# Kernel tuning notes

Hardware: AMD Instinct MI355X
Metric: run time of the kernel (lower is better)

Reference implementation:

```python
import jax, jax.numpy as jnp
import numpy as np

NUM_HEADS = 12   # top-k = num_heads experts selected per token
SWITCHLOSS = 0.1
ZLOSS = 0.001


def setup_inputs() -> dict:
    key = jax.random.key(0)
    ks = jax.random.split(key, 8)
    B, N, C, E, D = 2, 2048, 768, 24, 64
    w = lambda k, shape: (jax.random.normal(k, shape, jnp.float32) * 0.02)
    return {
        "x": jax.random.normal(ks[0], (B, N, C), jnp.float32),
        "w_gate": w(ks[1], (C, E)),
        "W_in": w(ks[2], (E, C, D)),    # per-expert q projection
        "b_in": jnp.zeros((E, D), jnp.float32),
        "W_out": w(ks[3], (E, D, C)),   # per-expert output projection
        "b_out": jnp.zeros((E, C), jnp.float32),
        "W_kv": w(ks[4], (C, 2 * D)),   # shared single-head K/V
        "b_kv": jnp.zeros((2 * D,), jnp.float32),
    }


def reference(x, w_gate, W_in, b_in, W_out, b_out, W_kv, b_kv):
    B, N, C = x.shape
    E, _, D = W_in.shape
    H = NUM_HEADS
    scale = D ** -0.5

    xf = x.reshape(-1, C)                         # [T, C], T = B*N
    # --- top-k gating (k = num_heads) ---
    logits = xf @ w_gate                          # [T, E]
    probs = jax.nn.softmax(logits, axis=-1)
    top_p, idx = jax.lax.top_k(probs, H)          # [T, H]
    gates = top_p / (top_p.sum(-1, keepdims=True) + 1e-6)
    oh = jax.nn.one_hot(idx, E, dtype=x.dtype)    # [T, H, E]
    comb = oh * gates[..., None]                  # gated dispatch/combine weights

    # --- aux losses (switchloss + zloss; cvloss coeff = 0) ---
    dense_gates = comb.sum(1)                     # [T, E]
    freqs = (dense_gates > 0).astype(x.dtype).sum(0)
    p_sum = probs.sum(0)
    switch = E * jnp.sum((p_sum / p_sum.sum()) * (freqs / freqs.sum()))
    z = jnp.mean(jax.nn.logsumexp(logits, axis=1) ** 2)
    aux_loss = SWITCHLOSS * switch + ZLOSS * z

    # --- MoE map: per-token q via selected experts (no gate multiply) ---
    q_all = jnp.einsum('tc,ecd->ted', xf, W_in) + b_in     # [T, E, D]
    q = jnp.take_along_axis(q_all, idx[..., None], axis=1)  # [T, H, D]
    q = q.reshape(B, N, H, D)

    # --- shared-KV attention (multi-query style) ---
    kv = x @ W_kv + b_kv
    k, v = jnp.split(kv, 2, axis=-1)              # [B, N, D] each
    attn = jnp.einsum('bihd,bjd->bhij', q, k) * scale
    attn = jax.nn.softmax(attn, axis=-1)
    o = jnp.einsum('bhij,bjd->bihd', attn, v).reshape(-1, H, D)  # [T, H, D]

    # --- MoE reduce: gated combine through per-expert output projections ---
    xe = jnp.einsum('the,thd->ted', comb, o)      # [T, E, D] gated dispatch
    out = jnp.einsum('ted,edc->tc', xe, W_out) + jnp.einsum('the,ec->tc', comb, b_out)
    return out.reshape(B, N, C), aux_loss
```

## Files before the change

### kernel.cpp

```cpp
#include <hip/hip_runtime.h>
#include <hip/hip_bf16.h>

#define T_  4096
#define Bb  2
#define Nn  2048
#define Cc  768
#define Ee  24
#define Dd  64
#define Hh  12
#define KR  1568
#define KS  16
#define KC  48
#define NB2 1024
#define SCL 0.18033688f

typedef __attribute__((ext_vector_type(8))) short bf16x8;
typedef __attribute__((ext_vector_type(4))) short bf16x4;
typedef __attribute__((ext_vector_type(4))) float f32x4;

__device__ __forceinline__ unsigned short f2bf(float f) {
  union { float f; unsigned int i; } u; u.f = f;
  unsigned int r = u.i + 0x7FFFu + ((u.i >> 16) & 1u);
  return (unsigned short)(r >> 16);
}
__device__ __forceinline__ float bf2f(unsigned short s) {
  union { unsigned int i; float f; } u; u.i = ((unsigned int)s) << 16; return u.f;
}

__device__ __forceinline__ void gload16(const void* g, void* l) {
  __builtin_amdgcn_global_load_lds(
      (const __attribute__((address_space(1))) void*)g,
      (__attribute__((address_space(3))) void*)l, 16, 0, 0);
}

__global__ __launch_bounds__(256) void convert_all_kernel(
    const float* __restrict__ W_in, const float* __restrict__ W_out,
    const float* __restrict__ b_out, const float* __restrict__ W_kv,
    unsigned short* __restrict__ BqT, unsigned short* __restrict__ BrT,
    unsigned short* __restrict__ BkvT)
{
  __shared__ float ls[64 * 129];
  const int bid = blockIdx.x, tid = threadIdx.x;
  if (bid < 288) {
    const int e = bid / 12, c0 = (bid % 12) * 64;
    #pragma unroll
    for (int i = 0; i < 16; ++i) {
      int L = tid + i * 256, c = L >> 6, d = L & 63;
      ls[c * 65 + d] = W_in[(size_t)e * Cc * Dd + (size_t)(c0 + c) * Dd + d];
    }
    __syncthreads();
    #pragma unroll
    for (int i = 0; i < 16; ++i) {
      int L = tid + i * 256, d = L >> 6, c = L & 63;
      BqT[(size_t)(e * Dd + d) * Cc + c0 + c] = f2bf(ls[c * 65 + d]);
    }
  } else if (bid < 876) {
    const int i2 = bid - 288;
    const int k0 = (i2 / 12) * 32, n0 = (i2 % 12) * 64;
    #pragma unroll
    for (int i = 0; i < 8; ++i) {
      int L = tid + i * 256, k = L >> 6, n = L & 63;
      int kk = k0 + k;
      float v = (kk < 1536) ? W_out[(size_t)kk * Cc + n0 + n]
              : (kk < 1560) ? b_out[(size_t)(kk - 1536) * Cc + n0 + n] : 0.f;
      ls[k * 65 + n] = v;
    }
    __syncthreads();
    #pragma unroll
    for (int i = 0; i < 8; ++i) {
      int L = tid + i * 256, n = L >> 5, k = L & 31;
      BrT[(size_t)(n0 + n) * KR + k0 + k] = f2bf(ls[k * 65 + n]);
    }
  } else {
    const int c0 = (bid - 876) * 64;
    #pragma unroll
    for (int i = 0; i < 32; ++i) {
      int L = tid + i * 256, c = L >> 7, j = L & 127;
      ls[c * 129 + j] = W_kv[(size_t)(c0 + c) * 128 + j];
    }
    __syncthreads();
    #pragma unroll
    for (int i = 0; i < 32; ++i) {
      int L = tid + i * 256, j = L >> 6, c = L & 63;
      BkvT[(size_t)j * Cc + c0 + c] = f2bf(ls[c * 129 + j]);
    }
  }
}

template<int MODE, int BM>
__global__ __launch_bounds__(256) void gemm_bt_kernel(
    const unsigned short* __restrict__ A, const unsigned short* __restrict__ BT,
    const float* __restrict__ bias, const float* __restrict__ bias2,
    void* __restrict__ Cout, void* __restrict__ Cout2, void* __restrict__ Cout3,
    int K, int ldc)
{
  constexpr int MI = BM / 32;
  __shared__ __align__(16) unsigned short As[BM * 32];
  __shared__ __align__(16) unsigned short Bs[128 * 32];
  const int tid = threadIdx.x, w = tid >> 6, lane = tid & 63;
  const int quad = lane >> 4, nl = lane & 15;
  const int m0 = blockIdx.x * BM, n0 = blockIdx.y * 128;
  const int mw = (w & 1) * (BM / 2), nw = (w >> 1) * 64;

  f32x4 acc[MI][4];
  #pragma unroll
  for (int i = 0; i < MI; ++i)
    #pragma unroll
    for (int j = 0; j < 4; ++j) acc[i][j] = (f32x4){0.f, 0.f, 0.f, 0.f};

  const int rlane = lane >> 2, col8 = (lane & 3) * 8;
  const int row0a = w * (BM / 4) + rlane;
  const int row0b = w * 32 + rlane;
  const unsigned short* a0 = A + (size_t)(m0 + row0a) * K + col8;
  const unsigned short* a1 = a0 + (size_t)16 * K;
  const unsigned short* b0 = BT + (size_t)(n0 + row0b) * K + col8;
  const unsigned short* b1 = b0 + (size_t)16 * K;
  unsigned short* lA0 = As + (w * (BM / 4)) * 32;
  unsigned short* lA1 = As + (w * (BM / 4) + 16) * 32;
  unsigned short* lB0 = Bs + (w * 32) * 32;
  unsigned short* lB1 = Bs + (w * 32 + 16) * 32;

  for (int k0 = 0; k0 < K; k0 += 32) {
    gload16(a0 + k0, lA0);
    if (BM == 128) gload16(a1 + k0, lA1);
    gload16(b0 + k0, lB0);
    gload16(b1 + k0, lB1);
    __syncthreads();

    bf16x8 af[MI], bfr[4];
    #pragma unroll
    for (int mi = 0; mi < MI; ++mi)
      af[mi] = *(const bf16x8*)&As[(mw + mi * 16 + nl) * 32 + quad * 8];
    #pragma unroll
    for (int ni = 0; ni < 4; ++ni)
      bfr[ni] = *(const bf16x8*)&Bs[(nw + ni * 16 + nl) * 32 + quad * 8];
    #pragma unroll
    for (int mi = 0; mi < MI; ++mi)
      #pragma unroll
      for (int ni = 0; ni < 4; ++ni)
        acc[mi][ni] = __builtin_amdgcn_mfma_f32_16x16x32_bf16(
            af[mi], bfr[ni], acc[mi][ni], 0, 0, 0);
    __syncthreads();
  }

  #pragma unroll
  for (int mi = 0; mi < MI; ++mi) {
    int rowb = m0 + mw + mi * 16 + quad * 4;
    int bb = rowb >> 11, nn = rowb & (Nn - 1);
    #pragma unroll
    for (int ni = 0; ni < 4; ++ni) {
      int col = n0 + nw + ni * 16 + nl;
      if (MODE == 0) {
        #pragma unroll
        for (int reg = 0; reg < 4; ++reg)
          ((float*)Cout)[(size_t)(rowb + reg) * ldc + col] = acc[mi][ni][reg];
      } else {
        if (col < 1536) {
          float bv = bias[col];
          #pragma unroll
          for (int reg = 0; reg < 4; ++reg)
            ((unsigned short*)Cout)[(size_t)(rowb + reg) * 1536 + col] =
                f2bf((acc[mi][ni][reg] + bv) * SCL);
        } else {
          int c2 = col - 1536;
          float bv = bias2[c2];
          if (c2 < Dd) {
            #pragma unroll
            for (int reg = 0; reg < 4; ++reg)
              ((unsigned short*)Cout2)[((size_t)bb * Nn + nn + reg) * Dd + c2] =
                  f2bf(acc[mi][ni][reg] + bv);
          } else {
            int p6 = nn & 63;
            int np = (nn & ~63) | (p6 & 0x23)
                   | (((p6 >> 4) & 1) << 2) | (((p6 >> 2) & 3) << 3);
            ushort4 v;
            v.x = f2bf(acc[mi][ni][0] + bv);
            v.y = f2bf(acc[mi][ni][1] + bv);
            v.z = f2bf(acc[mi][ni][2] + bv);
            v.w = f2bf(acc[mi][ni][3] + bv);
            *(ushort4*)((unsigned short*)Cout3 +
                        ((size_t)bb * Dd + (c2 - Dd)) * Nn + np) = v;
          }
        }
      }
    }
  }
}

#define XPAD 52
__global__ __launch_bounds__(256) void gate1_kernel(
    const float* __restrict__ x, const float* __restrict__ wg,
    float* __restrict__ partial, unsigned short* __restrict__ xb)
{
  __shared__ __align__(16) float xs[256 * XPAD];
  __shared__ __align__(16) float wsT[Ee * KC];
  const int tid = threadIdx.x;
  const int t0 = blockIdx.x * 256;
  const int s = blockIdx.y, k0 = s * KC;

  #pragma unroll
  for (int i = 0; i < 12; ++i) {
    int f = tid + i * 256;
    int token = f / 12, j = f % 12;
    size_t gofs = (size_t)(t0 + token) * Cc + k0 + j * 4;
    float4 v = *(const float4*)&x[gofs];
    *(float4*)&xs[token * XPAD + j * 4] = v;
    ushort4 o;
    o.x = f2bf(v.x); o.y = f2bf(v.y); o.z = f2bf(v.z); o.w = f2bf(v.w);
    *(ushort4*)&xb[gofs] = o;
  }
  for (int i = tid; i < Ee * KC; i += 256)
    wsT[(i % Ee) * KC + i / Ee] = wg[k0 * Ee + i];
  __syncthreads();

  float xr[KC];
  #pragma unroll
  for (int kg = 0; kg < KC / 4; ++kg)
    *(float4*)&xr[kg * 4] = *(const float4*)&xs[tid * XPAD + kg * 4];

  float acc[Ee];
  #pragma unroll
  for (int e = 0; e < Ee; ++e) acc[e] = 0.f;
  #pragma unroll
  for (int e = 0; e < Ee; ++e) {
    #pragma unroll
    for (int kg = 0; kg < KC / 4; ++kg) {
      float4 wv = *(const float4*)&wsT[e * KC + kg * 4];
      acc[e] += xr[kg * 4 + 0] * wv.x + xr[kg * 4 + 1] * wv.y
              + xr[kg * 4 + 2] * wv.z + xr[kg * 4 + 3] * wv.w;
    }
  }

  float* dst = partial + ((size_t)(t0 + tid) * KS + s) * Ee;
  #pragma unroll
  for (int eg = 0; eg < Ee / 4; ++eg)
    *(float4*)&dst[eg * 4] = *(float4*)&acc[eg * 4];
}

__global__ __launch_bounds__(256) void gate2_kernel(
    const float* __restrict__ partial,
    int* __restrict__ idx, float* __restrict__ gate, float* __restrict__ bstats)
{
  __shared__ float xls[4][KS * Ee];
  __shared__ float sacc[49];
  const int tid = threadIdx.x;
  const int w = tid >> 6, lane = tid & 63;
  const int t = blockIdx.x * 4 + w;

  if (tid < 49) sacc[tid] = 0.f;

  const float* p = partial + (size_t)t * (KS * Ee);
  #pragma unroll
  for (int i = 0; i < 6; ++i) xls[w][lane + i * 64] = p[lane + i * 64];

  float logit = -1e30f;
  if (lane < Ee) {
    float acc = 0.f;
    #pragma unroll
    for (int s = 0; s < KS; ++s) acc += xls[w][s * Ee + lane];
    logit = acc;
  }
  float m = logit;
  for (int o = 32; o; o >>= 1) m = fmaxf(m, __shfl_xor(m, o));
  float pr = (lane < Ee) ? expf(logit - m) : 0.f;
  float s = pr;
  for (int o = 32; o; o >>= 1) s += __shfl_xor(s, o);
  float prob = pr / s;
  float lse = m + logf(s);

  bool sel = false;
  float my_p = 0.f; int my_e = -1;
  for (int h = 0; h < Hh; ++h) {
    float v = (lane < Ee && !sel) ? prob : -1.f;
    int ix = lane;
    for (int o = 32; o; o >>= 1) {
      float ov = __shfl_xor(v, o); int oi = __shfl_xor(ix, o);
      if (ov > v || (ov == v && oi < ix)) { v = ov; ix = oi; }
    }
    if (lane == ix) sel = true;
    if (lane == h) { my_p = v; my_e = ix; }
  }
  float gsum = (lane < Hh) ? my_p : 0.f;
  for (int o = 32; o; o >>= 1) gsum += __shfl_xor(gsum, o);
  if (lane < Hh) {
    idx[t * Hh + lane] = my_e;
    gate[t * Hh + lane] = my_p / (gsum + 1e-6f);
  }

  __syncthreads();
  if (lane < Ee) atomicAdd(&sacc[lane], prob);
  if (lane < Hh) atomicAdd(&sacc[24 + my_e], 1.0f);
  if (lane == 0) atomicAdd(&sacc[48], lse * lse);
  __syncthreads();
  if (tid < 49) bstats[(size_t)tid * NB2 + blockIdx.x] = sacc[tid];
}

__global__ __launch_bounds__(256) void attn_kernel(
    const unsigned short* __restrict__ qallb, const int* __restrict__ idx,
    const unsigned short* __restrict__ kbuf, const unsigned short* __restrict__ vtbuf,
    float* __restrict__ opart, float* __restrict__ lpart)
{
  __shared__ __align__(16) unsigned short ksl[64 * 64];
  __shared__ __align__(16) unsigned short vtl[64 * 64];

  const int tid = threadIdx.x;
  const int w = tid >> 6, lane = tid & 63;
  const int quad = lane >> 4, nl = lane & 15;
  const int bh = blockIdx.y;
  const int b = bh / Hh, h = bh - b * Hh;
  const int qw = blockIdx.x * 128 + w * 32;
  const int sp = blockIdx.z;
  const int jbeg = sp * (Nn / 2);

  bf16x8 qB0[2], qB1[2];
  #pragma unroll
  for (int g = 0; g < 2; ++g) {
    const int tq = b * Nn + qw + g * 16 + nl;
    const int eq = idx[tq * Hh + h];
    const unsigned short* qrow = qallb + (size_t)tq * (Ee * Dd) + eq * Dd + quad * 8;
    qB0[g] = *(const bf16x8*)(qrow);
    qB1[g] = *(const bf16x8*)(qrow + 32);
  }

  f32x4 acc[2][4];
  #pragma unroll
  for (int g = 0; g < 2; ++g)
    #pragma unroll
    for (int dg = 0; dg < 4; ++dg) acc[g][dg] = (f32x4){0.f, 0.f, 0.f, 0.f};
  float l[2] = {0.f, 0.f};

  const int sr  = lane >> 3;
  const int cbd = (lane & 7) ^ sr;
  const int xl  = nl & 7;
  const int ca0 = (quad ^ xl) * 8;
  const int ca1 = ((quad + 4) ^ xl) * 8;

  for (int j0 = jbeg; j0 < jbeg + Nn / 2; j0 += 64) {
    #pragma unroll
    for (int i = 0; i < 2; ++i) {
      int r = w * 16 + i * 8;
      gload16(kbuf + ((size_t)b * Nn + j0 + r + sr) * Dd + cbd * 8, ksl + r * 64);
      gload16(vtbuf + ((size_t)b * Dd + r + sr) * Nn + j0 + cbd * 8, vtl + r * 64);
    }
    __syncthreads();

    bf16x4 pf[2][4];
    #pragma unroll
    for (int kg = 0; kg < 4; ++kg) {
      const unsigned short* kr = ksl + (kg * 16 + nl) * 64;
      bf16x8 a0 = *(const bf16x8*)(kr + ca0);
      bf16x8 a1 = *(const bf16x8*)(kr + ca1);
      #pragma unroll
      for (int g = 0; g < 2; ++g) {
        f32x4 c = {0.f, 0.f, 0.f, 0.f};
        c = __builtin_amdgcn_mfma_f32_16x16x32_bf16(a0, qB0[g], c, 0, 0, 0);
        c = __builtin_amdgcn_mfma_f32_16x16x32_bf16(a1, qB1[g], c, 0, 0, 0);
        float p0 = __builtin_amdgcn_exp2f(c[0]);
        float p1 = __builtin_amdgcn_exp2f(c[1]);
        float p2 = __builtin_amdgcn_exp2f(c[2]);
        float p3 = __builtin_amdgcn_exp2f(c[3]);
        l[g] += (p0 + p1) + (p2 + p3);
        union { __hip_bfloat162 h2[2]; bf16x4 v; } pk;
        pk.h2[0] = __float22bfloat162_rn(float2{p0, p1});
        pk.h2[1] = __float22bfloat162_rn(float2{p2, p3});
        pf[g][kg] = pk.v;
      }
    }
    bf16x8 pb[2][2];
    #pragma unroll
    for (int g = 0; g < 2; ++g) {
      pb[g][0] = __builtin_shufflevector(pf[g][0], pf[g][1], 0, 1, 2, 3, 4, 5, 6, 7);
      pb[g][1] = __builtin_shufflevector(pf[g][2], pf[g][3], 0, 1, 2, 3, 4, 5, 6, 7);
    }
    #pragma unroll
    for (int dg = 0; dg < 4; ++dg) {
      const unsigned short* vrow = vtl + (dg * 16 + nl) * 64;
      bf16x8 v0 = *(const bf16x8*)(vrow + ca0);
      bf16x8 v1 = *(const bf16x8*)(vrow + ca1);
      #pragma unroll
      for (int g = 0; g < 2; ++g) {
        acc[g][dg] = __builtin_amdgcn_mfma_f32_16x16x32_bf16(v0, pb[g][0], acc[g][dg], 0, 0, 0);
        acc[g][dg] = __builtin_amdgcn_mfma_f32_16x16x32_bf16(v1, pb[g][1], acc[g][dg], 0, 0, 0);
      }
    }
    __syncthreads();
  }

  #pragma unroll
  for (int g = 0; g < 2; ++g) {
    float lg = l[g];
    lg += __shfl_xor(lg, 16);
    lg += __shfl_xor(lg, 32);
    if (lane < 16)
      lpart[(size_t)sp * (Bb * Hh * Nn) + (size_t)bh * Nn + qw + g * 16 + nl] = lg;
    float* orow = opart + (size_t)sp * ((size_t)Bb * Hh * Nn * Dd)
                + ((size_t)bh * Nn + qw + g * 16 + nl) * Dd + quad * 4;
    #pragma unroll
    for (int dg = 0; dg < 4; ++dg) {
      float4 o;
      o.x = acc[g][dg][0]; o.y = acc[g][dg][1];
      o.z = acc[g][dg][2]; o.w = acc[g][dg][3];
      *(float4*)(orow + dg * 16) = o;
    }
  }
}

__global__ __launch_bounds__(256) void scatter_kernel(
    const float* __restrict__ opart, const float* __restrict__ lpart,
    const int* __restrict__ idx, const float* __restrict__ gate,
    unsigned short* __restrict__ xeg)
{
  __shared__ int   sel[Ee];
  __shared__ float glh[Hh];
  __shared__ float gg[Hh];
  const int t = blockIdx.x, b = t >> 11, nn = t & (Nn - 1);
  const int tid = threadIdx.x;
  const size_t HN = (size_t)Bb * Hh * Nn;
  if (tid < Ee) sel[tid] = -1;
  __syncthreads();
  if (tid < Hh) {
    int e = idx[t * Hh + tid];
    sel[e] = tid;
    float g = gate[t * Hh + tid];
    gg[tid] = g;
    size_t row = (size_t)(b * Hh + tid) * Nn + nn;
    glh[tid] = g / (lpart[row] + lpart[HN + row]);
  }
  __syncthreads();
  for (int c = tid; c < KR; c += 256) {
    float v = 0.f;
    if (c < 1536) {
      int e = c >> 6, h = sel[e];
      if (h >= 0) {
        size_t oofs = ((size_t)(b * Hh + h) * Nn + nn) * Dd + (c & 63);
        v = glh[h] * (opart[oofs] + opart[HN * Dd + oofs]);
      }
    } else if (c < 1560) {
      int h = sel[c - 1536];
      if (h >= 0) v = gg[h];
    }
    xeg[(size_t)t * KR + c] = f2bf(v);
  }
}

__global__ __launch_bounds__(256) void aux1_kernel(
    const float* __restrict__ bstats, float* __restrict__ stats2)
{
  __shared__ float r[4];
  const int j = blockIdx.x, tid = threadIdx.x;
  float4 v = *(const float4*)&bstats[(size_t)j * NB2 + tid * 4];
  float s = (v.x + v.y) + (v.z + v.w);
  for (int o = 32; o; o >>= 1) s += __shfl_xor(s, o);
  if ((tid & 63) == 0) r[tid >> 6] = s;
  __syncthreads();
  if (tid == 0) stats2[j] = (r[0] + r[1]) + (r[2] + r[3]);
}

__global__ void aux2_kernel(const float* __restrict__ stats2,
                            float* __restrict__ out, int out_size)
{
  const int lane = threadIdx.x;
  float a = (lane < Ee) ? stats2[lane] : 0.f;
  float b = (lane < Ee) ? stats2[24 + lane] : 0.f;
  float pt = a, ft = b, sw = a * b;
  for (int o = 32; o; o >>= 1) {
    pt += __shfl_xor(pt, o); ft += __shfl_xor(ft, o); sw += __shfl_xor(sw, o);
  }
  if (lane == 0) {
    float sswitch = (float)Ee * sw / (pt * ft);
    float z = stats2[48] * (1.0f / (float)T_);
    out[out_size - 1] = 0.1f * sswitch + 0.001f * z;
  }
}

extern "C" void kernel_launch(void* const* d_in, const int* in_sizes, int n_in,
                              void* d_out, int out_size, void* d_ws, size_t ws_size,
                              hipStream_t stream)
{
  const float* x     = (const float*)d_in[0];
  const float* wg    = (const float*)d_in[1];
  const float* W_in  = (const float*)d_in[2];
  const float* b_in  = (const float*)d_in[3];
  const float* W_out = (const float*)d_in[4];
  const float* b_out = (const float*)d_in[5];
  const float* W_kv  = (const float*)d_in[6];
  const float* b_kv  = (const float*)d_in[7];
  float* out = (float*)d_out;

  char* ws = (char*)d_ws;
  size_t off = 0;
  auto carve = [&](size_t bytes) -> void* {
    void* p = ws + off;
    off = (off + bytes + 255) & ~(size_t)255;
    return p;
  };
  int*            idx    = (int*)           carve((size_t)T_ * Hh * 4);
  float*          gate   = (float*)         carve((size_t)T_ * Hh * 4);
  float*          bstats = (float*)         carve((size_t)49 * NB2 * 4);
  float*          stats2 = (float*)         carve(256);
  float*          lpart  = (float*)         carve((size_t)2 * Bb * Hh * Nn * 4);
  float*          lgate  = (float*)         carve((size_t)T_ * KS * Ee * 4);
  unsigned short* xb     = (unsigned short*)carve((size_t)T_ * Cc * 2);
  unsigned short* BqkvT  = (unsigned short*)carve((size_t)(Ee * Dd + 128) * Cc * 2);
  unsigned short* BkvT   = BqkvT + (size_t)Ee * Dd * Cc;
  unsigned short* BrT    = (unsigned short*)carve((size_t)Cc * KR * 2);
  unsigned short* kbuf   = (unsigned short*)carve((size_t)T_ * Dd * 2);
  unsigned short* vtbuf  = (unsigned short*)carve((size_t)T_ * Dd * 2);
  unsigned short* qallb  = (unsigned short*)carve((size_t)T_ * Ee * Dd * 2);
  float*          opart  = (float*)         carve((size_t)2 * Bb * Hh * Nn * Dd * 4);
  unsigned short* xeg    = (unsigned short*)carve((size_t)T_ * KR * 2);

  convert_all_kernel<<<888, 256, 0, stream>>>(
      W_in, W_out, b_out, W_kv, BqkvT, BrT, BkvT);

  gate1_kernel<<<dim3(T_ / 256, KS), 256, 0, stream>>>(x, wg, lgate, xb);
  gate2_kernel<<<NB2, 256, 0, stream>>>(lgate, idx, gate, bstats);

  gemm_bt_kernel<1, 64><<<dim3(T_ / 64, 13), 256, 0, stream>>>(
      xb, BqkvT, b_in, b_kv, qallb, kbuf, vtbuf, Cc, 1536);

  attn_kernel<<<dim3(Nn / 128, Bb * Hh, 2), 256, 0, stream>>>(
      qallb, idx, kbuf, vtbuf, opart, lpart);

  scatter_kernel<<<T_, 256, 0, stream>>>(opart, lpart, idx, gate, xeg);

  gemm_bt_kernel<0, 64><<<dim3(T_ / 64, Cc / 128), 256, 0, stream>>>(
      xeg, BrT, nullptr, nullptr, out, nullptr, nullptr, KR, Cc);

  aux1_kernel<<<49, 256, 0, stream>>>(bstats, stats2);
  aux2_kernel<<<1, 64, 0, stream>>>(stats2, out, out_size);
}
```

Before: 215.3 us.

## Triple-buffer K/V tiles in attention and enlarge GEMM row tiles

The attention kernel now keeps three LDS buffers for K and V^T tiles. It issues asynchronous loads two tiles ahead and waits on partial vmcnt counts, so global loads overlap MFMA compute. It also raises wave priority during compute and sets launch bounds to 3 blocks per CU. Separately, both GEMM launches switch to 128-row tiles, which halves the grid size and gives more reuse per block, at the cost of fewer blocks and more LDS and registers.

```diff
diff --git a/kernel.cpp b/kernel.cpp
--- a/kernel.cpp
+++ b/kernel.cpp
@@ -295,13 +295,13 @@
   if (tid < 49) bstats[(size_t)tid * NB2 + blockIdx.x] = sacc[tid];
 }
 
-__global__ __launch_bounds__(256) void attn_kernel(
+__global__ __launch_bounds__(256, 3) void attn_kernel(
     const unsigned short* __restrict__ qallb, const int* __restrict__ idx,
     const unsigned short* __restrict__ kbuf, const unsigned short* __restrict__ vtbuf,
     float* __restrict__ opart, float* __restrict__ lpart)
 {
-  __shared__ __align__(16) unsigned short ksl[64 * 64];
-  __shared__ __align__(16) unsigned short vtl[64 * 64];
+  __shared__ __align__(16) unsigned short ksl[3][64 * 64];
+  __shared__ __align__(16) unsigned short vtl[3][64 * 64];
 
   const int tid = threadIdx.x;
   const int w = tid >> 6, lane = tid & 63;
@@ -310,7 +310,7 @@
   const int b = bh / Hh, h = bh - b * Hh;
   const int qw = blockIdx.x * 128 + w * 32;
   const int sp = blockIdx.z;
-  const int jbeg = sp * (Nn / 2);
+  const int T0 = sp * 16;
 
   bf16x8 qB0[2], qB1[2];
   #pragma unroll
@@ -335,19 +335,26 @@
   const int ca0 = (quad ^ xl) * 8;
   const int ca1 = ((quad + 4) ^ xl) * 8;
 
-  for (int j0 = jbeg; j0 < jbeg + Nn / 2; j0 += 64) {
+  const unsigned short* kgbase =
+      kbuf + ((size_t)b * Nn + w * 16 + sr) * Dd + cbd * 8;
+  const unsigned short* vgbase =
+      vtbuf + ((size_t)b * Dd + w * 16 + sr) * Nn + cbd * 8;
+
+  auto STAGE = [&](int bi, int t) {
+    const int j0 = t * 64;
     #pragma unroll
     for (int i = 0; i < 2; ++i) {
-      int r = w * 16 + i * 8;
-      gload16(kbuf + ((size_t)b * Nn + j0 + r + sr) * Dd + cbd * 8, ksl + r * 64);
-      gload16(vtbuf + ((size_t)b * Dd + r + sr) * Nn + j0 + cbd * 8, vtl + r * 64);
-    }
-    __syncthreads();
-
+      gload16(kgbase + (size_t)(j0 + i * 8) * Dd, &ksl[bi][(w * 16 + i * 8) * 64]);
+      gload16(vgbase + (size_t)(i * 8) * Nn + j0, &vtl[bi][(w * 16 + i * 8) * 64]);
+    }
+  };
+
+  auto COMPUTE = [&](const unsigned short* ks_, const unsigned short* vt_) {
+    __builtin_amdgcn_s_setprio(1);
     bf16x4 pf[2][4];
     #pragma unroll
     for (int kg = 0; kg < 4; ++kg) {
-      const unsigned short* kr = ksl + (kg * 16 + nl) * 64;
+      const unsigned short* kr = ks_ + (kg * 16 + nl) * 64;
       bf16x8 a0 = *(const bf16x8*)(kr + ca0);
       bf16x8 a1 = *(const bf16x8*)(kr + ca1);
       #pragma unroll
@@ -374,7 +381,7 @@
     }
     #pragma unroll
     for (int dg = 0; dg < 4; ++dg) {
-      const unsigned short* vrow = vtl + (dg * 16 + nl) * 64;
+      const unsigned short* vrow = vt_ + (dg * 16 + nl) * 64;
       bf16x8 v0 = *(const bf16x8*)(vrow + ca0);
       bf16x8 v1 = *(const bf16x8*)(vrow + ca1);
       #pragma unroll
@@ -383,8 +390,39 @@
         acc[g][dg] = __builtin_amdgcn_mfma_f32_16x16x32_bf16(v1, pb[g][1], acc[g][dg], 0, 0, 0);
       }
     }
-    __syncthreads();
-  }
+    __builtin_amdgcn_s_setprio(0);
+  };
+
+#define PIPE8(SB, ST, CB)                                   \
+    STAGE(SB, ST);                                          \
+    asm volatile("s_waitcnt vmcnt(8)" ::: "memory");        \
+    __builtin_amdgcn_s_barrier();                           \
+    __builtin_amdgcn_sched_barrier(0);                      \
+    COMPUTE(ksl[CB], vtl[CB]);                              \
+    __builtin_amdgcn_sched_barrier(0);                      \
+    asm volatile("" ::: "memory");                          \
+    __builtin_amdgcn_s_barrier();
+
+  STAGE(0, T0 + 0);
+  STAGE(1, T0 + 1);
+  #pragma unroll 1
+  for (int t = 0; t < 12; t += 3) {
+    PIPE8(2, T0 + t + 2, 0);
+    PIPE8(0, T0 + t + 3, 1);
+    PIPE8(1, T0 + t + 4, 2);
+  }
+  PIPE8(2, T0 + 14, 0);
+  PIPE8(0, T0 + 15, 1);
+  asm volatile("s_waitcnt vmcnt(4)" ::: "memory");
+  __builtin_amdgcn_s_barrier();
+  __builtin_amdgcn_sched_barrier(0);
+  COMPUTE(ksl[2], vtl[2]);
+  __builtin_amdgcn_sched_barrier(0);
+  asm volatile("s_waitcnt vmcnt(0)" ::: "memory");
+  __builtin_amdgcn_s_barrier();
+  __builtin_amdgcn_sched_barrier(0);
+  COMPUTE(ksl[0], vtl[0]);
+#undef PIPE8
 
   #pragma unroll
   for (int g = 0; g < 2; ++g) {
@@ -516,7 +554,7 @@
   gate1_kernel<<<dim3(T_ / 256, KS), 256, 0, stream>>>(x, wg, lgate, xb);
   gate2_kernel<<<NB2, 256, 0, stream>>>(lgate, idx, gate, bstats);
 
-  gemm_bt_kernel<1, 64><<<dim3(T_ / 64, 13), 256, 0, stream>>>(
+  gemm_bt_kernel<1, 128><<<dim3(T_ / 128, 13), 256, 0, stream>>>(
       xb, BqkvT, b_in, b_kv, qallb, kbuf, vtbuf, Cc, 1536);
 
   attn_kernel<<<dim3(Nn / 128, Bb * Hh, 2), 256, 0, stream>>>(
@@ -524,7 +562,7 @@
 
   scatter_kernel<<<T_, 256, 0, stream>>>(opart, lpart, idx, gate, xeg);
 
-  gemm_bt_kernel<0, 64><<<dim3(T_ / 64, Cc / 128), 256, 0, stream>>>(
+  gemm_bt_kernel<0, 128><<<dim3(T_ / 128, Cc / 128), 256, 0, stream>>>(
       xeg, BrT, nullptr, nullptr, out, nullptr, nullptr, KR, Cc);
 
   aux1_kernel<<<49, 256, 0, stream>>>(bstats, stats2);
```

Result: slower. 235.4 us (+9.3%).
